# Kernel tuning notes

Measured on AMD Instinct MI355X. Metric: run time of the kernel, lower is better.

## Reference

```python
import jax, jax.numpy as jnp
import numpy as np

IN_F = 4096
OUT_F = 4096
SPARSITY = 0.9
NNZ = round((1.0 - SPARSITY) * IN_F * OUT_F)  # 1677722
BATCH = 4096


def setup_inputs() -> dict:
    key = jax.random.key(0)
    k1, k2, k3, k4 = jax.random.split(key, 4)
    x = jax.random.normal(k1, (BATCH, IN_F), dtype=jnp.float32)
    # Kaiming-ish scale for sparse fan-in
    weights = jax.random.normal(k2, (NNZ,), dtype=jnp.float32) * 0.02
    row = jax.random.randint(k3, (NNZ,), 0, OUT_F, dtype=jnp.int32)
    col = jax.random.randint(k4, (NNZ,), 0, IN_F, dtype=jnp.int32)
    indices = jnp.stack([row, col], axis=0)  # (2, nnz) like the torch buffer
    active_mask = jnp.ones((NNZ,), dtype=bool)
    return {
        "x": x,
        "weights": weights,
        "indices": indices,
        "active_mask": active_mask,
        "out_features": OUT_F,
        "in_features": IN_F,
    }


def reference(x, weights, indices, active_mask, out_features, in_features):
    # Torch forward: select active edges, build COO (out,in), coalesce
    # (sums duplicate indices), then y = (W @ x^T)^T.
    # Equivalent math: zero inactive weights, scatter-add into dense W,
    # then a dense matmul. Duplicates are summed by .add, matching coalesce.
    w = jnp.where(active_mask, weights, jnp.zeros((), dtype=weights.dtype))
    W = jnp.zeros((out_features, in_features), dtype=x.dtype)
    W = W.at[indices[0], indices[1]].add(w)  # (out, in)
    return x @ W.T  # (B, out)
```

## Files before the change

### kernel.cpp

```cpp
#include <hip/hip_runtime.h>
#include <cstdint>
#include <cstddef>

#define IN_F  4096
#define OUT_F 4096
#define BATCH 4096

typedef __bf16 bf16_t;
typedef __bf16 bf16x8 __attribute__((ext_vector_type(8)));
typedef float  f32x4  __attribute__((ext_vector_type(4)));

__device__ __forceinline__ unsigned short f32_to_bf16_rne(float f) {
  union { float f; unsigned int u; } v;
  v.f = f;
  unsigned int u = v.u;
  return (unsigned short)((u + 0x7FFFu + ((u >> 16) & 1u)) >> 16);
}

__device__ __forceinline__ uint4 cvt8(float4 a, float4 b) {
  uint4 o;
  o.x = (unsigned)f32_to_bf16_rne(a.x) | ((unsigned)f32_to_bf16_rne(a.y) << 16);
  o.y = (unsigned)f32_to_bf16_rne(a.z) | ((unsigned)f32_to_bf16_rne(a.w) << 16);
  o.z = (unsigned)f32_to_bf16_rne(b.x) | ((unsigned)f32_to_bf16_rne(b.y) << 16);
  o.w = (unsigned)f32_to_bf16_rne(b.z) | ((unsigned)f32_to_bf16_rne(b.w) << 16);
  return o;
}

#define XUNITS ((BATCH * IN_F) / 8)

__global__ __launch_bounds__(256) void scatter_cvtx(
    const float* __restrict__ w, const int* __restrict__ rows,
    const int* __restrict__ cols, const int* __restrict__ mask,
    unsigned* __restrict__ Wpk, int nnz,
    const float4* __restrict__ xin, uint4* __restrict__ xbf) {
  const int total = XUNITS + nnz;
  for (int u = blockIdx.x * 256 + threadIdx.x; u < total;
       u += gridDim.x * 256) {
    if (u < nnz) {
      if (mask[u] != 0) {
        const unsigned h = f32_to_bf16_rne(w[u]);
        const size_t e = (size_t)rows[u] * IN_F + cols[u];
        const unsigned data = (e & 1) ? (h << 16) : h;
        unsigned* p = Wpk + (e >> 1);
        asm volatile("global_atomic_pk_add_bf16 %0, %1, off"
                     :: "v"(p), "v"(data) : "memory");
      }
    } else {
      const int i = u - nnz;
      xbf[i] = cvt8(xin[2 * i], xin[2 * i + 1]);
    }
  }
}

#define A0_B 0
#define B0_B 32768
#define A1_B 65536
#define B1_B 98304
#define HALF 16384

#define STAGE(Xg, kpos, ldsbase) do {                                          \
  __builtin_amdgcn_global_load_lds(                                            \
    (const __attribute__((address_space(1))) void*)((Xg) + (size_t)srow * 4096 + (kpos) + schunk), \
    (__attribute__((address_space(3))) void*)(lds + (ldsbase) + tid * 16), 16, 0, 0); \
  __builtin_amdgcn_global_load_lds(                                            \
    (const __attribute__((address_space(1))) void*)((Xg) + (size_t)(srow + 128) * 4096 + (kpos) + schunk), \
    (__attribute__((address_space(3))) void*)(lds + (ldsbase) + 8192 + tid * 16), 16, 0, 0); \
} while (0)

#define RDB(base) do {                                                         \
  _Pragma("unroll")                                                            \
  for (int ni = 0; ni < 4; ++ni)                                               \
    _Pragma("unroll")                                                          \
    for (int kk = 0; kk < 2; ++kk)                                             \
      b[ni][kk] = *(const bf16x8*)(lds + (base) + kk * HALF + offB[ni]);       \
} while (0)

#define RDA(base, q) do {                                                      \
  _Pragma("unroll")                                                            \
  for (int mi = 0; mi < 2; ++mi)                                               \
    _Pragma("unroll")                                                          \
    for (int kk = 0; kk < 2; ++kk)                                             \
      a[mi][kk] = *(const bf16x8*)(lds + (base) + kk * HALF + offA[q][mi]);    \
} while (0)

#define MFMAQ(q) do {                                                          \
  _Pragma("unroll")                                                            \
  for (int mi = 0; mi < 2; ++mi)                                               \
    _Pragma("unroll")                                                          \
    for (int ni = 0; ni < 4; ++ni)                                             \
      _Pragma("unroll")                                                        \
      for (int kk = 0; kk < 2; ++kk)                                           \
        acc[2 * (q) + mi][ni] = __builtin_amdgcn_mfma_f32_16x16x32_bf16(       \
            a[mi][kk], b[ni][kk], acc[2 * (q) + mi][ni], 0, 0, 0);             \
} while (0)

#define BAR()   __builtin_amdgcn_s_barrier()
#define LGKM0() do { asm volatile("s_waitcnt lgkmcnt(0)" ::: "memory");        \
                     __builtin_amdgcn_sched_barrier(0); } while (0)
#define VM(n)   asm volatile("s_waitcnt vmcnt(" #n ")" ::: "memory")
#define PRIO1() __builtin_amdgcn_s_setprio(1)
#define PRIO0() __builtin_amdgcn_s_setprio(0)

__global__ __launch_bounds__(512, 2) void gemm_q(
    const bf16_t* __restrict__ A, const bf16_t* __restrict__ Bm,
    float* __restrict__ C) {
  __shared__ __align__(16) char lds[131072];

  const int tid  = threadIdx.x;
  const int lane = tid & 63;
  const int wave = tid >> 6;
  const int wm   = wave >> 2;
  const int wn   = wave & 3;

  const int sbid = (blockIdx.x & 7) * 32 + (blockIdx.x >> 3);
  const int bm   = sbid >> 4;
  const int bn   = sbid & 15;

  const int frow = lane & 15;
  const int c16  = (lane >> 4) * 16;

  int offA[4][2], offB[4];
#pragma unroll
  for (int q = 0; q < 4; ++q)
#pragma unroll
    for (int mi = 0; mi < 2; ++mi) {
      int r = wm * 128 + q * 32 + mi * 16 + frow;
      offA[q][mi] = r * 64 + (c16 ^ (((r >> 1) & 3) << 4));
    }
#pragma unroll
  for (int ni = 0; ni < 4; ++ni) {
    int r = wn * 64 + ni * 16 + frow;
    offB[ni] = r * 64 + (c16 ^ (((r >> 1) & 3) << 4));
  }

  const int srow   = tid >> 2;
  const int schunk = ((tid & 3) ^ ((srow >> 1) & 3)) * 8;
  const bf16_t* Ag = A  + (size_t)bm * 256 * 4096;
  const bf16_t* Bg = Bm + (size_t)bn * 256 * 4096;

  f32x4 acc[8][4] = {};
  bf16x8 a[2][2], b[4][2];

  STAGE(Ag, 0,  A0_B);
  STAGE(Ag, 32, A0_B + HALF);
  STAGE(Bg, 0,  B0_B);
  STAGE(Bg, 32, B0_B + HALF);
  STAGE(Bg, 64, B1_B);
  STAGE(Bg, 96, B1_B + HALF);
  VM(4);
  BAR();

  int kb = 0;
#pragma unroll 1
  for (int i = 0; i < 31; ++i, kb += 128) {
    RDB(B0_B); RDA(A0_B, 0);
    STAGE(Ag, kb + 64, A1_B);
    BAR(); LGKM0(); PRIO1(); MFMAQ(0); PRIO0(); BAR();
    RDA(A0_B, 1);
    STAGE(Ag, kb + 96, A1_B + HALF);
    BAR(); LGKM0(); PRIO1(); MFMAQ(1); PRIO0(); BAR();
    RDA(A0_B, 2);
    STAGE(Bg, kb + 128, B0_B);
    BAR(); LGKM0(); PRIO1(); MFMAQ(2); PRIO0(); BAR();
    RDA(A0_B, 3);
    STAGE(Bg, kb + 160, B0_B + HALF);
    BAR(); LGKM0(); PRIO1(); MFMAQ(3); PRIO0(); VM(4); BAR();
    RDB(B1_B); RDA(A1_B, 0);
    STAGE(Ag, kb + 128, A0_B);
    BAR(); LGKM0(); PRIO1(); MFMAQ(0); PRIO0(); BAR();
    RDA(A1_B, 1);
    STAGE(Ag, kb + 160, A0_B + HALF);
    BAR(); LGKM0(); PRIO1(); MFMAQ(1); PRIO0(); BAR();
    RDA(A1_B, 2);
    STAGE(Bg, kb + 192, B1_B);
    BAR(); LGKM0(); PRIO1(); MFMAQ(2); PRIO0(); BAR();
    RDA(A1_B, 3);
    STAGE(Bg, kb + 224, B1_B + HALF);
    BAR(); LGKM0(); PRIO1(); MFMAQ(3); PRIO0(); VM(4); BAR();
  }

  RDB(B0_B); RDA(A0_B, 0);
  STAGE(Ag, 4032, A1_B);
  BAR(); LGKM0(); PRIO1(); MFMAQ(0); PRIO0(); BAR();
  RDA(A0_B, 1);
  STAGE(Ag, 4064, A1_B + HALF);
  BAR(); LGKM0(); PRIO1(); MFMAQ(1); PRIO0(); BAR();
  RDA(A0_B, 2);
  BAR(); LGKM0(); PRIO1(); MFMAQ(2); PRIO0(); BAR();
  RDA(A0_B, 3);
  BAR(); LGKM0(); PRIO1(); MFMAQ(3); PRIO0(); VM(0); BAR();
  RDB(B1_B); RDA(A1_B, 0);
  BAR(); LGKM0(); PRIO1(); MFMAQ(0); PRIO0(); BAR();
  RDA(A1_B, 1);
  BAR(); LGKM0(); PRIO1(); MFMAQ(1); PRIO0(); BAR();
  RDA(A1_B, 2);
  BAR(); LGKM0(); PRIO1(); MFMAQ(2); PRIO0(); BAR();
  RDA(A1_B, 3);
  LGKM0(); PRIO1(); MFMAQ(3); PRIO0();

#pragma unroll
  for (int m = 0; m < 8; ++m)
#pragma unroll
    for (int ni = 0; ni < 4; ++ni) {
      const int row = bm * 256 + wm * 128 + m * 16 + (lane >> 4) * 4;
      const int col = bn * 256 + wn * 64 + ni * 16 + frow;
#pragma unroll
      for (int jj = 0; jj < 4; ++jj)
        C[(size_t)(row + jj) * 4096 + col] = acc[m][ni][jj];
    }
}

extern "C" void kernel_launch(void* const* d_in, const int* in_sizes, int n_in,
                              void* d_out, int out_size, void* d_ws, size_t ws_size,
                              hipStream_t stream) {
  const float* x     = (const float*)d_in[0];
  const float* wvals = (const float*)d_in[1];
  const int*   idx   = (const int*)d_in[2];
  const int*   mk    = (const int*)d_in[3];
  const int    nnz   = in_sizes[1];

  bf16_t* Wbf = (bf16_t*)d_ws;
  bf16_t* xbf = (bf16_t*)((char*)d_ws + (size_t)OUT_F * IN_F * sizeof(bf16_t));

  const size_t needed = (size_t)OUT_F * IN_F * 2 + (size_t)BATCH * IN_F * 2;
  if (ws_size < needed) return;

  hipMemsetAsync(Wbf, 0, (size_t)OUT_F * IN_F * sizeof(bf16_t), stream);

  scatter_cvtx<<<2048, 256, 0, stream>>>(
      wvals, idx, idx + nnz, mk, (unsigned*)Wbf, nnz,
      (const float4*)x, (uint4*)xbf);

  gemm_q<<<256, 512, 0, stream>>>(xbf, Wbf, (float*)d_out);
}
```

Before: 198.9 us.

## Switch GEMM to 32x32x16 MFMA with 128-byte-row swizzled LDS layout

Replaces the 16x16x32 bf16 MFMA tiles with 32x32x16 MFMA. The LDS layout changes from two 64-byte K-halves to one 128-byte row per tile row, with an 8-way XOR swizzle, and the staging, fragment offsets and epilogue store mapping are rewritten to match. The larger MFMA shape needs fewer LDS fragment reads per flop and fewer instructions issued. In exchange it brings a different register footprint and a new bank-conflict pattern.

```diff
diff --git a/kernel.cpp b/kernel.cpp
--- a/kernel.cpp
+++ b/kernel.cpp
@@ -8,7 +8,7 @@
 
 typedef __bf16 bf16_t;
 typedef __bf16 bf16x8 __attribute__((ext_vector_type(8)));
-typedef float  f32x4  __attribute__((ext_vector_type(4)));
+typedef float  f32x16 __attribute__((ext_vector_type(16)));
 
 __device__ __forceinline__ unsigned short f32_to_bf16_rne(float f) {
   union { float f; unsigned int u; } v;
@@ -56,42 +56,37 @@
 #define B0_B 32768
 #define A1_B 65536
 #define B1_B 98304
-#define HALF 16384
-
-#define STAGE(Xg, kpos, ldsbase) do {                                          \
+
+#define STAGE(Xg, kpos, ldsbase, roff) do {                                    \
   __builtin_amdgcn_global_load_lds(                                            \
-    (const __attribute__((address_space(1))) void*)((Xg) + (size_t)srow * 4096 + (kpos) + schunk), \
-    (__attribute__((address_space(3))) void*)(lds + (ldsbase) + tid * 16), 16, 0, 0); \
+    (const __attribute__((address_space(1))) void*)((Xg) + (size_t)(srow + (roff)) * 4096 + (kpos) + schunk), \
+    (__attribute__((address_space(3))) void*)(lds + (ldsbase) + (roff) * 128 + tid * 16), 16, 0, 0); \
   __builtin_amdgcn_global_load_lds(                                            \
-    (const __attribute__((address_space(1))) void*)((Xg) + (size_t)(srow + 128) * 4096 + (kpos) + schunk), \
-    (__attribute__((address_space(3))) void*)(lds + (ldsbase) + 8192 + tid * 16), 16, 0, 0); \
+    (const __attribute__((address_space(1))) void*)((Xg) + (size_t)(srow + (roff) + 64) * 4096 + (kpos) + schunk), \
+    (__attribute__((address_space(3))) void*)(lds + (ldsbase) + (roff) * 128 + 8192 + tid * 16), 16, 0, 0); \
 } while (0)
 
 #define RDB(base) do {                                                         \
   _Pragma("unroll")                                                            \
-  for (int ni = 0; ni < 4; ++ni)                                               \
+  for (int ni = 0; ni < 2; ++ni)                                               \
     _Pragma("unroll")                                                          \
-    for (int kk = 0; kk < 2; ++kk)                                             \
-      b[ni][kk] = *(const bf16x8*)(lds + (base) + kk * HALF + offB[ni]);       \
+    for (int kk = 0; kk < 4; ++kk)                                             \
+      b[ni][kk] = *(const bf16x8*)(lds + (base) + offB[ni][kk]);               \
 } while (0)
 
 #define RDA(base, q) do {                                                      \
   _Pragma("unroll")                                                            \
-  for (int mi = 0; mi < 2; ++mi)                                               \
-    _Pragma("unroll")                                                          \
-    for (int kk = 0; kk < 2; ++kk)                                             \
-      a[mi][kk] = *(const bf16x8*)(lds + (base) + kk * HALF + offA[q][mi]);    \
+  for (int kk = 0; kk < 4; ++kk)                                               \
+    a[kk] = *(const bf16x8*)(lds + (base) + offA[q][kk]);                      \
 } while (0)
 
 #define MFMAQ(q) do {                                                          \
   _Pragma("unroll")                                                            \
-  for (int mi = 0; mi < 2; ++mi)                                               \
+  for (int kk = 0; kk < 4; ++kk)                                               \
     _Pragma("unroll")                                                          \
-    for (int ni = 0; ni < 4; ++ni)                                             \
-      _Pragma("unroll")                                                        \
-      for (int kk = 0; kk < 2; ++kk)                                           \
-        acc[2 * (q) + mi][ni] = __builtin_amdgcn_mfma_f32_16x16x32_bf16(       \
-            a[mi][kk], b[ni][kk], acc[2 * (q) + mi][ni], 0, 0, 0);             \
+    for (int ni = 0; ni < 2; ++ni)                                             \
+      acc[q][ni] = __builtin_amdgcn_mfma_f32_32x32x16_bf16(                    \
+          a[kk], b[ni][kk], acc[q][ni], 0, 0, 0);                              \
 } while (0)
 
 #define BAR()   __builtin_amdgcn_s_barrier()
@@ -101,7 +96,7 @@
 #define PRIO1() __builtin_amdgcn_s_setprio(1)
 #define PRIO0() __builtin_amdgcn_s_setprio(0)
 
-__global__ __launch_bounds__(512, 2) void gemm_q(
+__global__ __launch_bounds__(512, 2) void gemm_q32(
     const bf16_t* __restrict__ A, const bf16_t* __restrict__ Bm,
     float* __restrict__ C) {
   __shared__ __align__(16) char lds[131072];
@@ -116,37 +111,36 @@
   const int bm   = sbid >> 4;
   const int bn   = sbid & 15;
 
-  const int frow = lane & 15;
-  const int c16  = (lane >> 4) * 16;
-
-  int offA[4][2], offB[4];
+  const int l31 = lane & 31;
+  const int hi  = lane >> 5;
+
+  int offA[4][4], offB[2][4];
 #pragma unroll
   for (int q = 0; q < 4; ++q)
 #pragma unroll
-    for (int mi = 0; mi < 2; ++mi) {
-      int r = wm * 128 + q * 32 + mi * 16 + frow;
-      offA[q][mi] = r * 64 + (c16 ^ (((r >> 1) & 3) << 4));
-    }
-#pragma unroll
-  for (int ni = 0; ni < 4; ++ni) {
-    int r = wn * 64 + ni * 16 + frow;
-    offB[ni] = r * 64 + (c16 ^ (((r >> 1) & 3) << 4));
-  }
-
-  const int srow   = tid >> 2;
-  const int schunk = ((tid & 3) ^ ((srow >> 1) & 3)) * 8;
+    for (int kk = 0; kk < 4; ++kk) {
+      const int r = wm * 128 + q * 32 + l31;
+      offA[q][kk] = r * 128 + (((kk * 2 + hi) ^ ((r >> 1) & 7)) << 4);
+    }
+#pragma unroll
+  for (int ni = 0; ni < 2; ++ni)
+#pragma unroll
+    for (int kk = 0; kk < 4; ++kk) {
+      const int r = wn * 64 + ni * 32 + l31;
+      offB[ni][kk] = r * 128 + (((kk * 2 + hi) ^ ((r >> 1) & 7)) << 4);
+    }
+
+  const int srow   = tid >> 3;
+  const int schunk = ((tid & 7) ^ ((srow >> 1) & 7)) * 8;
   const bf16_t* Ag = A  + (size_t)bm * 256 * 4096;
   const bf16_t* Bg = Bm + (size_t)bn * 256 * 4096;
 
-  f32x4 acc[8][4] = {};
-  bf16x8 a[2][2], b[4][2];
-
-  STAGE(Ag, 0,  A0_B);
-  STAGE(Ag, 32, A0_B + HALF);
-  STAGE(Bg, 0,  B0_B);
-  STAGE(Bg, 32, B0_B + HALF);
-  STAGE(Bg, 64, B1_B);
-  STAGE(Bg, 96, B1_B + HALF);
+  f32x16 acc[4][2] = {};
+  bf16x8 a[4], b[2][4];
+
+  STAGE(Ag, 0,  A0_B, 0);  STAGE(Ag, 0,  A0_B, 128);
+  STAGE(Bg, 0,  B0_B, 0);  STAGE(Bg, 0,  B0_B, 128);
+  STAGE(Bg, 64, B1_B, 0);  STAGE(Bg, 64, B1_B, 128);
   VM(4);
   BAR();
 
@@ -154,36 +148,36 @@
 #pragma unroll 1
   for (int i = 0; i < 31; ++i, kb += 128) {
     RDB(B0_B); RDA(A0_B, 0);
-    STAGE(Ag, kb + 64, A1_B);
+    STAGE(Ag, kb + 64, A1_B, 0);
     BAR(); LGKM0(); PRIO1(); MFMAQ(0); PRIO0(); BAR();
     RDA(A0_B, 1);
-    STAGE(Ag, kb + 96, A1_B + HALF);
+    STAGE(Ag, kb + 64, A1_B, 128);
     BAR(); LGKM0(); PRIO1(); MFMAQ(1); PRIO0(); BAR();
     RDA(A0_B, 2);
-    STAGE(Bg, kb + 128, B0_B);
+    STAGE(Bg, kb + 128, B0_B, 0);
     BAR(); LGKM0(); PRIO1(); MFMAQ(2); PRIO0(); BAR();
     RDA(A0_B, 3);
-    STAGE(Bg, kb + 160, B0_B + HALF);
+    STAGE(Bg, kb + 128, B0_B, 128);
     BAR(); LGKM0(); PRIO1(); MFMAQ(3); PRIO0(); VM(4); BAR();
     RDB(B1_B); RDA(A1_B, 0);
-    STAGE(Ag, kb + 128, A0_B);
+    STAGE(Ag, kb + 128, A0_B, 0);
     BAR(); LGKM0(); PRIO1(); MFMAQ(0); PRIO0(); BAR();
     RDA(A1_B, 1);
-    STAGE(Ag, kb + 160, A0_B + HALF);
+    STAGE(Ag, kb + 128, A0_B, 128);
     BAR(); LGKM0(); PRIO1(); MFMAQ(1); PRIO0(); BAR();
     RDA(A1_B, 2);
-    STAGE(Bg, kb + 192, B1_B);
+    STAGE(Bg, kb + 192, B1_B, 0);
     BAR(); LGKM0(); PRIO1(); MFMAQ(2); PRIO0(); BAR();
     RDA(A1_B, 3);
-    STAGE(Bg, kb + 224, B1_B + HALF);
+    STAGE(Bg, kb + 192, B1_B, 128);
     BAR(); LGKM0(); PRIO1(); MFMAQ(3); PRIO0(); VM(4); BAR();
   }
 
   RDB(B0_B); RDA(A0_B, 0);
-  STAGE(Ag, 4032, A1_B);
+  STAGE(Ag, 4032, A1_B, 0);
   BAR(); LGKM0(); PRIO1(); MFMAQ(0); PRIO0(); BAR();
   RDA(A0_B, 1);
-  STAGE(Ag, 4064, A1_B + HALF);
+  STAGE(Ag, 4032, A1_B, 128);
   BAR(); LGKM0(); PRIO1(); MFMAQ(1); PRIO0(); BAR();
   RDA(A0_B, 2);
   BAR(); LGKM0(); PRIO1(); MFMAQ(2); PRIO0(); BAR();
@@ -199,14 +193,16 @@
   LGKM0(); PRIO1(); MFMAQ(3); PRIO0();
 
 #pragma unroll
-  for (int m = 0; m < 8; ++m)
-#pragma unroll
-    for (int ni = 0; ni < 4; ++ni) {
-      const int row = bm * 256 + wm * 128 + m * 16 + (lane >> 4) * 4;
-      const int col = bn * 256 + wn * 64 + ni * 16 + frow;
-#pragma unroll
-      for (int jj = 0; jj < 4; ++jj)
-        C[(size_t)(row + jj) * 4096 + col] = acc[m][ni][jj];
+  for (int q = 0; q < 4; ++q)
+#pragma unroll
+    for (int ni = 0; ni < 2; ++ni) {
+      const int rbase = bm * 256 + wm * 128 + q * 32 + 4 * hi;
+      const int col   = bn * 256 + wn * 64 + ni * 32 + l31;
+#pragma unroll
+      for (int reg = 0; reg < 16; ++reg) {
+        const int row = rbase + (reg & 3) + 8 * (reg >> 2);
+        C[(size_t)row * 4096 + col] = acc[q][ni][reg];
+      }
     }
 }
 
@@ -231,5 +227,5 @@
       wvals, idx, idx + nnz, mk, (unsigned*)Wbf, nnz,
       (const float4*)x, (uint4*)xbf);
 
-  gemm_q<<<256, 512, 0, stream>>>(xbf, Wbf, (float*)d_out);
-}
+  gemm_q32<<<256, 512, 0, stream>>>(xbf, Wbf, (float*)d_out);
+}
```

New measurement: 204.6 us. 1.03x slower.
